# Performance work log

Measured on AMD Instinct MI355X. Metric: run time of the kernel, lower is better.

The kernel has to match this reference:

```python
import jax, jax.numpy as jnp
import numpy as np

B, S, E, H = 2, 2048, 1024, 16
D = E // H  # head_dim = 64


def setup_inputs() -> dict:
    key = jax.random.key(0)
    k1, k2, k3 = jax.random.split(key, 3)
    scale = 0.02  # GPT-2 init scale
    return {
        "hidden_states": jax.random.normal(k1, (B, S, E), dtype=jnp.float32),
        "c_attn_w": jax.random.normal(k2, (E, 3 * E), dtype=jnp.float32) * scale,
        "c_attn_b": jnp.zeros((3 * E,), dtype=jnp.float32),
        "c_proj_w": jax.random.normal(k3, (E, E), dtype=jnp.float32) * scale,
        "c_proj_b": jnp.zeros((E,), dtype=jnp.float32),
    }


def reference(hidden_states, c_attn_w, c_attn_b, c_proj_w, c_proj_b):
    # Conv1D: x @ W + b  -> qkv [B, S, 3E]
    qkv = hidden_states @ c_attn_w + c_attn_b
    q, k, v = jnp.split(qkv, 3, axis=-1)

    # split heads -> [B, H, S, D]
    def split_heads(t):
        return t.reshape(B, S, H, D).transpose(0, 2, 1, 3)

    q, k, v = split_heads(q), split_heads(k), split_heads(v)

    # naive full attention: QK^T / sqrt(D) -> softmax -> @ V
    attn_weights = jnp.einsum("bhqd,bhkd->bhqk", q, k) / jnp.sqrt(
        jnp.asarray(D, dtype=q.dtype)
    )
    attn_weights = jax.nn.softmax(attn_weights, axis=-1)
    attn_output = jnp.einsum("bhqk,bhkd->bhqd", attn_weights, v)

    # merge heads -> [B, S, E], then output projection
    attn_output = attn_output.transpose(0, 2, 1, 3).reshape(B, S, E)
    attn_output = attn_output @ c_proj_w + c_proj_b
    return attn_output
```

## Files before the change

kernel.cpp:

```cpp
#include <hip/hip_runtime.h>

#define SEQ 2048
#define EMB 1024
#define KDIM 1024
#define CF 0.180336880111113f

typedef __attribute__((ext_vector_type(8))) short short8_t;
typedef __attribute__((ext_vector_type(4))) float floatx4;
typedef __attribute__((ext_vector_type(4))) unsigned short ushort4_t;
typedef __attribute__((ext_vector_type(4))) unsigned int uivec4;

#define GLOAD16(gp, lp)                                                        \
  __builtin_amdgcn_global_load_lds(                                            \
      (const __attribute__((address_space(1))) void*)(gp),                     \
      (__attribute__((address_space(3))) void*)(lp), 16, 0, 0)

#define WGBAR()                                   \
  do {                                            \
    __asm__ __volatile__("" ::: "memory");        \
    __builtin_amdgcn_s_barrier();                 \
    __asm__ __volatile__("" ::: "memory");        \
  } while (0)

static __device__ __forceinline__ unsigned short f2bf(float x) {
  unsigned int u = __float_as_uint(x);
  return (unsigned short)((u + 0x7fffu + ((u >> 16) & 1u)) >> 16);
}

static __device__ __forceinline__ short8_t mk_pb(unsigned int a, unsigned int b,
                                                 unsigned int c, unsigned int d) {
  uivec4 t;
  t[0] = a; t[1] = b; t[2] = c; t[3] = d;
  return __builtin_bit_cast(short8_t, t);
}

static __device__ __forceinline__ unsigned int pack_bf(float p0, float p1) {
  return __builtin_amdgcn_perm(__float_as_uint(p1), __float_as_uint(p0),
                               0x07060302u);
}

static __device__ __forceinline__ void tconv_tile(
    const float* __restrict__ W, unsigned short* __restrict__ T, int N, int K,
    int n0, int k0, int tid) {
  __shared__ float Tl[64][65];
  const int lx = tid & 15, ly = tid >> 4;
#pragma unroll
  for (int u = 0; u < 4; ++u) {
    int r = u * 16 + ly;
    float4 v = *(const float4*)&W[(size_t)(k0 + r) * N + n0 + lx * 4];
    Tl[r][lx * 4 + 0] = v.x;
    Tl[r][lx * 4 + 1] = v.y;
    Tl[r][lx * 4 + 2] = v.z;
    Tl[r][lx * 4 + 3] = v.w;
  }
  __syncthreads();
#pragma unroll
  for (int u = 0; u < 4; ++u) {
    int n = u * 16 + ly;
    ushort4_t h;
#pragma unroll
    for (int v = 0; v < 4; ++v) h[v] = f2bf(Tl[lx * 4 + v][n]);
    *(ushort4_t*)&T[(size_t)(n0 + n) * K + k0 + lx * 4] = h;
  }
}

__global__ __launch_bounds__(256) void prep(
    const float* __restrict__ hs, const float* __restrict__ caw,
    const float* __restrict__ cpw, unsigned short* __restrict__ hsb,
    unsigned short* __restrict__ w1t, unsigned short* __restrict__ w2t) {
  const int bid = blockIdx.x, tid = threadIdx.x;
  if (bid < 4096) {
    const int i = bid * 256 + tid;
    float4 v = *(const float4*)&hs[(size_t)i * 4];
    ushort4_t h = {f2bf(v.x), f2bf(v.y), f2bf(v.z), f2bf(v.w)};
    *(ushort4_t*)&hsb[(size_t)i * 4] = h;
  } else if (bid < 4864) {
    const int idx = bid - 4096;
    tconv_tile(caw, w1t, 3 * EMB, EMB, (idx % 48) * 64, (idx / 48) * 64, tid);
  } else {
    const int idx = bid - 4864;
    tconv_tile(cpw, w2t, EMB, EMB, (idx % 16) * 64, (idx / 16) * 64, tid);
  }
}

template <int MODE, int BN>
__global__ __launch_bounds__(256, MODE == 0 ? 2 : 3) void gemm_pl(
    const unsigned short* __restrict__ Ag, const unsigned short* __restrict__ Bg,
    const float* __restrict__ bias, float* __restrict__ outF,
    unsigned short* __restrict__ qk, unsigned short* __restrict__ vt) {
  __shared__ __attribute__((aligned(16))) unsigned short Ah[2][128 * 64];
  __shared__ __attribute__((aligned(16))) unsigned short Bh[2][BN * 64];
  const int NJ = BN / 32;

  const int tid = threadIdx.x;
  const int w = tid >> 6, lane = tid & 63;
  const int quad = lane >> 4, c = lane & 15;
  const int rk = c & 7;

  int bm, bn;
  {
    const int L = blockIdx.x, x = L & 7, g = L >> 3;
    if (MODE == 0) {
      bm = ((x & 1) * 16 + (g & 15)) * 128;
      bn = ((x >> 1) * 6 + (g >> 4)) * 128;
    } else {
      bm = ((x & 3) * 8 + (g & 7)) * 128;
      bn = ((x >> 2) * 8 + (g >> 3)) * 64;
    }
  }
  const int wm = (w >> 1) * 64, wn = (w & 1) * (BN / 2);

  const unsigned short* gsrc = (w < 2) ? Ag : Bg;
  const int lbo = (w < 2) ? (w & 1) * 64 * 64 : (w & 1) * (BN / 2) * 64;
  const int rbase = (w < 2) ? (bm + (w & 1) * 64) : (bn + (w & 1) * (BN / 2));
  const int nloads = (w < 2) ? 8 : (BN / 16);
  const int srow = lane >> 3;
  const int sblkg = (lane & 7) ^ srow;
  const char* gp0 = (const char*)(gsrc + (size_t)(rbase + srow) * KDIM) + sblkg * 16;

  floatx4 acc[4][NJ];
  const floatx4 z = {0.f, 0.f, 0.f, 0.f};
#pragma unroll
  for (int i = 0; i < 4; ++i)
#pragma unroll
    for (int j = 0; j < NJ; ++j) acc[i][j] = z;

#define STAGE_G(buf, kt)                                                       \
  do {                                                                         \
    unsigned short* ld = ((w < 2) ? Ah[buf] : Bh[buf]) + lbo;                  \
    const char* gp = gp0 + (size_t)(kt) * 128;                                 \
    for (int i_ = 0; i_ < nloads; ++i_)                                        \
      GLOAD16(gp + (size_t)i_ * 8 * (KDIM * 2), &ld[i_ * 512]);                \
  } while (0)

  STAGE_G(0, 0);

  for (int t = 0; t < 16; ++t) {
    __asm__ __volatile__("s_waitcnt vmcnt(0)" ::: "memory");
    WGBAR();
    if (t < 15) STAGE_G((t + 1) & 1, t + 1);
    const unsigned short* Ac = Ah[t & 1];
    const unsigned short* Bc = Bh[t & 1];

#pragma unroll
    for (int kd = 0; kd < 2; ++kd) {
      const int oct = ((4 * kd + quad) ^ rk) * 8;
      short8_t a[4], b[NJ];
#pragma unroll
      for (int i = 0; i < 4; ++i)
        a[i] = *(const short8_t*)&Ac[(wm + 16 * i + c) * 64 + oct];
#pragma unroll
      for (int j = 0; j < NJ; ++j)
        b[j] = *(const short8_t*)&Bc[(wn + 16 * j + c) * 64 + oct];
#pragma unroll
      for (int i = 0; i < 4; ++i)
#pragma unroll
        for (int j = 0; j < NJ; ++j)
          acc[i][j] = __builtin_amdgcn_mfma_f32_16x16x32_bf16(b[j], a[i], acc[i][j], 0, 0, 0);
    }
  }
#undef STAGE_G

#pragma unroll
  for (int i = 0; i < 4; ++i) {
    const int row = bm + wm + 16 * i + c;
#pragma unroll
    for (int j = 0; j < NJ; ++j) {
      const int col0 = bn + wn + 16 * j + quad * 4;
      floatx4 v = acc[i][j] + *(const floatx4*)&bias[col0];
      if (MODE == 0) {
        if (col0 < 1024) v = v * CF;
        if (col0 < 2048) {
          ushort4_t pk = {f2bf(v[0]), f2bf(v[1]), f2bf(v[2]), f2bf(v[3])};
          *(ushort4_t*)&qk[(size_t)row * 2048 + col0] = pk;
        } else {
          const int c2 = col0 - 2048, hh = c2 >> 6, d0 = c2 & 63;
          const int bb = row >> 11, s = row & 2047;
          const int j = s & 63;
          const int lam = (j & 0x20) | ((j & 0x0C) << 1) | ((j & 0x10) >> 2) | (j & 3);
          const int sp = (s & ~63) | lam;
          unsigned short* vb = &vt[((size_t)(bb * 16 + hh) * 64 + d0) * 2048 + sp];
          vb[0 * 2048] = f2bf(v[0]);
          vb[1 * 2048] = f2bf(v[1]);
          vb[2 * 2048] = f2bf(v[2]);
          vb[3 * 2048] = f2bf(v[3]);
        }
      } else {
        *(floatx4*)&outF[(size_t)row * 1024 + col0] = v;
      }
    }
  }
}

static __device__ __forceinline__ void stage_kv16(
    int w, int srow, int sblkg, const unsigned short* __restrict__ gK,
    const unsigned short* __restrict__ gV, unsigned short* Kbuf,
    unsigned short* Vbuf, int jt) {
  if (w < 4) {
    const unsigned short* g0 =
        gK + (size_t)(jt * 64 + w * 16 + srow) * 2048 + sblkg * 8;
    unsigned short* l0 = &Kbuf[(w * 16) * 64];
    GLOAD16(g0, l0);
    GLOAD16(g0 + (size_t)8 * 2048, l0 + 8 * 64);
  } else {
    const unsigned short* g0 =
        gV + (size_t)((w - 4) * 16 + srow) * 2048 + jt * 64 + sblkg * 8;
    unsigned short* l0 = &Vbuf[((w - 4) * 16) * 64];
    GLOAD16(g0, l0);
    GLOAD16(g0 + (size_t)8 * 2048, l0 + 8 * 64);
  }
}

__global__ __launch_bounds__(512, 1) void attn10(
    const unsigned short* __restrict__ qk, const unsigned short* __restrict__ vt,
    unsigned short* __restrict__ ao) {
  __shared__ __attribute__((aligned(16))) unsigned short KV[6 * 4096];
  unsigned short* Ksb = KV;
  unsigned short* Vsb = KV + 3 * 4096;

  const int tid = threadIdx.x;
  const int w = tid >> 6, lane = tid & 63, quad = lane >> 4, c = lane & 15;
  const int qh = w >> 1, kh = w & 1;
  const int L = blockIdx.x, x = L & 7, g = L >> 3;
  const int hb = x * 4 + (g >> 3);
  const int h = hb & 15, b = hb >> 4;
  const int q0 = (g & 7) * 256;
  const int rk = c & 7;

  short8_t qf[4][2];
  {
    const size_t rb = (size_t)b * SEQ + q0 + qh * 64;
#pragma unroll
    for (int mi = 0; mi < 4; ++mi) {
      const size_t qr = (rb + mi * 16 + c) * 2048 + h * 64 + quad * 8;
      qf[mi][0] = *(const short8_t*)&qk[qr];
      qf[mi][1] = *(const short8_t*)&qk[qr + 32];
    }
  }
  __asm__ __volatile__("s_waitcnt vmcnt(0)" ::: "memory");

  floatx4 O[4][4], Osum[4];
  const floatx4 z = {0.f, 0.f, 0.f, 0.f};
#pragma unroll
  for (int mi = 0; mi < 4; ++mi) {
    Osum[mi] = z;
#pragma unroll
    for (int dg = 0; dg < 4; ++dg) O[mi][dg] = z;
  }
  short8_t ones;
#pragma unroll
  for (int e = 0; e < 8; ++e) ones[e] = (short)0x3F80;

  const int srow = lane >> 3;
  const int sblkg = (lane & 7) ^ srow;
  const unsigned short* gK = qk + (size_t)b * SEQ * 2048 + 1024 + h * 64;
  const unsigned short* gV = vt + (size_t)(b * 16 + h) * 64 * 2048;

  stage_kv16(w, srow, sblkg, gK, gV, Ksb, Vsb, 0);
  stage_kv16(w, srow, sblkg, gK, gV, Ksb + 4096, Vsb + 4096, 1);

  const int octv = ((4 * kh + quad) ^ rk) * 8;

  for (int t = 0; t < 32; ++t) {
    __asm__ __volatile__("s_waitcnt vmcnt(2)" ::: "memory");
    WGBAR();
    stage_kv16(w, srow, sblkg, gK, gV, Ksb + ((t + 2) % 3) * 4096,
               Vsb + ((t + 2) % 3) * 4096, (t + 2) & 31);
    const unsigned short* Kc = Ksb + (t % 3) * 4096;
    const unsigned short* Vc = Vsb + (t % 3) * 4096;

    floatx4 S[4][2];
#pragma unroll
    for (int mi = 0; mi < 4; ++mi)
#pragma unroll
      for (int jg = 0; jg < 2; ++jg) S[mi][jg] = z;
#pragma unroll
    for (int kd = 0; kd < 2; ++kd) {
      const int oct = ((4 * kd + quad) ^ rk) * 8;
#pragma unroll
      for (int jg = 0; jg < 2; ++jg) {
        short8_t kf = *(const short8_t*)&Kc[((kh * 2 + jg) * 16 + c) * 64 + oct];
#pragma unroll
        for (int mi = 0; mi < 4; ++mi)
          S[mi][jg] = __builtin_amdgcn_mfma_f32_16x16x32_bf16(kf, qf[mi][kd], S[mi][jg], 0, 0, 0);
      }
    }

#pragma unroll
    for (int mi = 0; mi < 4; ++mi) {
      unsigned int pw[2][2];
#pragma unroll
      for (int jg = 0; jg < 2; ++jg) {
        float p0 = __builtin_amdgcn_exp2f(S[mi][jg][0]);
        float p1 = __builtin_amdgcn_exp2f(S[mi][jg][1]);
        float p2 = __builtin_amdgcn_exp2f(S[mi][jg][2]);
        float p3 = __builtin_amdgcn_exp2f(S[mi][jg][3]);
        pw[jg][0] = pack_bf(p0, p1);
        pw[jg][1] = pack_bf(p2, p3);
      }
      short8_t pb = mk_pb(pw[0][0], pw[0][1], pw[1][0], pw[1][1]);
      Osum[mi] = __builtin_amdgcn_mfma_f32_16x16x32_bf16(ones, pb, Osum[mi], 0, 0, 0);
#pragma unroll
      for (int dg = 0; dg < 4; ++dg) {
        short8_t vf = *(const short8_t*)&Vc[(dg * 16 + c) * 64 + octv];
        O[mi][dg] = __builtin_amdgcn_mfma_f32_16x16x32_bf16(vf, pb, O[mi][dg], 0, 0, 0);
      }
    }
  }

  __asm__ __volatile__("s_waitcnt vmcnt(0)" ::: "memory");
  WGBAR();

  float* Of = (float*)KV;
  float* Ss2 = (float*)((char*)KV + 34816);
#pragma unroll
  for (int p = 0; p < 2; ++p) {
    if (kh == 1 && (qh >> 1) == p) {
#pragma unroll
      for (int mi = 0; mi < 4; ++mi) {
        const int row = (qh & 1) * 64 + mi * 16 + c;
        float* orow = &Of[row * 68];
#pragma unroll
        for (int dg = 0; dg < 4; ++dg)
          *(floatx4*)&orow[dg * 16 + quad * 4] = O[mi][dg];
        if (quad == 0) Ss2[row] = Osum[mi][0];
      }
    }
    WGBAR();
    if (kh == 0 && (qh >> 1) == p) {
#pragma unroll
      for (int mi = 0; mi < 4; ++mi) {
        const int row = (qh & 1) * 64 + mi * 16 + c;
        const float inv = 1.0f / (Osum[mi][0] + Ss2[row]);
        const float* orow = &Of[row * 68];
        const size_t grow = (size_t)b * SEQ + q0 + qh * 64 + mi * 16 + c;
#pragma unroll
        for (int dg = 0; dg < 4; ++dg) {
          floatx4 o = O[mi][dg] + *(const floatx4*)&orow[dg * 16 + quad * 4];
          ushort4_t ov = {f2bf(o[0] * inv), f2bf(o[1] * inv),
                          f2bf(o[2] * inv), f2bf(o[3] * inv)};
          *(ushort4_t*)&ao[grow * EMB + h * 64 + dg * 16 + quad * 4] = ov;
        }
      }
    }
    WGBAR();
  }
}

extern "C" void kernel_launch(void* const* d_in, const int* in_sizes, int n_in,
                              void* d_out, int out_size, void* d_ws, size_t ws_size,
                              hipStream_t stream) {
  const float* hs = (const float*)d_in[0];
  const float* c_attn_w = (const float*)d_in[1];
  const float* c_attn_b = (const float*)d_in[2];
  const float* c_proj_w = (const float*)d_in[3];
  const float* c_proj_b = (const float*)d_in[4];
  float* out = (float*)d_out;

  char* ws = (char*)d_ws;
  unsigned short* hsb = (unsigned short*)(ws + 0);
  unsigned short* qk  = (unsigned short*)(ws + 8388608);
  unsigned short* vt  = (unsigned short*)(ws + 25165824);
  unsigned short* aob = (unsigned short*)(ws + 33554432);
  unsigned short* w1t = (unsigned short*)(ws + 41943040);
  unsigned short* w2t = (unsigned short*)(ws + 48234496);

  prep<<<5120, 256, 0, stream>>>(hs, c_attn_w, c_proj_w, hsb, w1t, w2t);
  gemm_pl<0, 128><<<768, 256, 0, stream>>>(hsb, w1t, c_attn_b, nullptr, qk, vt);
  attn10<<<256, 512, 0, stream>>>(qk, vt, aob);
  gemm_pl<2, 64><<<512, 256, 0, stream>>>(aob, w2t, c_proj_b, out, nullptr, nullptr);
}
```

Before: 169.7 us.

## Give each warp private K staging and direct V register loads, removing block barriers

Restructures the attention kernel so each of the 8 warps owns 32 query rows and walks all keys on its own. Each warp streams K through a private triple-buffered LDS region and loads V straight from global memory into double-buffered registers. This removes the block-wide barriers and the cross-warp reduction of partial O and row sums at the end. In exchange, each warp fetches K and V itself, so global and L2 traffic per block goes up roughly eightfold, and the smaller per-warp MFMA tiles reuse each loaded K/V fragment less.

```diff
diff --git a/kernel.cpp b/kernel.cpp
--- a/kernel.cpp
+++ b/kernel.cpp
@@ -192,57 +192,32 @@
   }
 }
 
-static __device__ __forceinline__ void stage_kv16(
-    int w, int srow, int sblkg, const unsigned short* __restrict__ gK,
-    const unsigned short* __restrict__ gV, unsigned short* Kbuf,
-    unsigned short* Vbuf, int jt) {
-  if (w < 4) {
-    const unsigned short* g0 =
-        gK + (size_t)(jt * 64 + w * 16 + srow) * 2048 + sblkg * 8;
-    unsigned short* l0 = &Kbuf[(w * 16) * 64];
-    GLOAD16(g0, l0);
-    GLOAD16(g0 + (size_t)8 * 2048, l0 + 8 * 64);
-  } else {
-    const unsigned short* g0 =
-        gV + (size_t)((w - 4) * 16 + srow) * 2048 + jt * 64 + sblkg * 8;
-    unsigned short* l0 = &Vbuf[((w - 4) * 16) * 64];
-    GLOAD16(g0, l0);
-    GLOAD16(g0 + (size_t)8 * 2048, l0 + 8 * 64);
-  }
-}
-
-__global__ __launch_bounds__(512, 1) void attn10(
+__global__ __launch_bounds__(512, 1) void attn12(
     const unsigned short* __restrict__ qk, const unsigned short* __restrict__ vt,
     unsigned short* __restrict__ ao) {
-  __shared__ __attribute__((aligned(16))) unsigned short KV[6 * 4096];
-  unsigned short* Ksb = KV;
-  unsigned short* Vsb = KV + 3 * 4096;
+  __shared__ __attribute__((aligned(16))) unsigned short Kpriv[8 * 3 * 2048];
 
   const int tid = threadIdx.x;
   const int w = tid >> 6, lane = tid & 63, quad = lane >> 4, c = lane & 15;
-  const int qh = w >> 1, kh = w & 1;
   const int L = blockIdx.x, x = L & 7, g = L >> 3;
   const int hb = x * 4 + (g >> 3);
   const int h = hb & 15, b = hb >> 4;
-  const int q0 = (g & 7) * 256;
+  const int q0 = (g & 7) * 256 + w * 32;
   const int rk = c & 7;
 
-  short8_t qf[4][2];
-  {
-    const size_t rb = (size_t)b * SEQ + q0 + qh * 64;
-#pragma unroll
-    for (int mi = 0; mi < 4; ++mi) {
-      const size_t qr = (rb + mi * 16 + c) * 2048 + h * 64 + quad * 8;
-      qf[mi][0] = *(const short8_t*)&qk[qr];
-      qf[mi][1] = *(const short8_t*)&qk[qr + 32];
-    }
+  short8_t qf[2][2];
+#pragma unroll
+  for (int mi = 0; mi < 2; ++mi) {
+    const size_t qr = ((size_t)(b * SEQ + q0 + mi * 16 + c)) * 2048 + h * 64 + quad * 8;
+    qf[mi][0] = *(const short8_t*)&qk[qr];
+    qf[mi][1] = *(const short8_t*)&qk[qr + 32];
   }
   __asm__ __volatile__("s_waitcnt vmcnt(0)" ::: "memory");
 
-  floatx4 O[4][4], Osum[4];
+  floatx4 O[2][4], Osum[2];
   const floatx4 z = {0.f, 0.f, 0.f, 0.f};
 #pragma unroll
-  for (int mi = 0; mi < 4; ++mi) {
+  for (int mi = 0; mi < 2; ++mi) {
     Osum[mi] = z;
 #pragma unroll
     for (int dg = 0; dg < 4; ++dg) O[mi][dg] = z;
@@ -255,95 +230,95 @@
   const int sblkg = (lane & 7) ^ srow;
   const unsigned short* gK = qk + (size_t)b * SEQ * 2048 + 1024 + h * 64;
   const unsigned short* gV = vt + (size_t)(b * 16 + h) * 64 * 2048;
-
-  stage_kv16(w, srow, sblkg, gK, gV, Ksb, Vsb, 0);
-  stage_kv16(w, srow, sblkg, gK, gV, Ksb + 4096, Vsb + 4096, 1);
-
-  const int octv = ((4 * kh + quad) ^ rk) * 8;
-
-  for (int t = 0; t < 32; ++t) {
-    __asm__ __volatile__("s_waitcnt vmcnt(2)" ::: "memory");
-    WGBAR();
-    stage_kv16(w, srow, sblkg, gK, gV, Ksb + ((t + 2) % 3) * 4096,
-               Vsb + ((t + 2) % 3) * 4096, (t + 2) & 31);
-    const unsigned short* Kc = Ksb + (t % 3) * 4096;
-    const unsigned short* Vc = Vsb + (t % 3) * 4096;
-
-    floatx4 S[4][2];
-#pragma unroll
-    for (int mi = 0; mi < 4; ++mi)
-#pragma unroll
-      for (int jg = 0; jg < 2; ++jg) S[mi][jg] = z;
-#pragma unroll
-    for (int kd = 0; kd < 2; ++kd) {
-      const int oct = ((4 * kd + quad) ^ rk) * 8;
-#pragma unroll
-      for (int jg = 0; jg < 2; ++jg) {
-        short8_t kf = *(const short8_t*)&Kc[((kh * 2 + jg) * 16 + c) * 64 + oct];
-#pragma unroll
-        for (int mi = 0; mi < 4; ++mi)
-          S[mi][jg] = __builtin_amdgcn_mfma_f32_16x16x32_bf16(kf, qf[mi][kd], S[mi][jg], 0, 0, 0);
-      }
+  unsigned short* Kb = &Kpriv[w * 3 * 2048];
+
+#define STK(buf, t)                                                            \
+  do {                                                                         \
+    const unsigned short* g0_ = gK + (size_t)((t) * 32 + srow) * 2048 + sblkg * 8; \
+    unsigned short* l0_ = Kb + (buf) * 2048;                                   \
+    GLOAD16(g0_, l0_);                                                         \
+    GLOAD16(g0_ + (size_t)8 * 2048, l0_ + 512);                                \
+    GLOAD16(g0_ + (size_t)16 * 2048, l0_ + 1024);                              \
+    GLOAD16(g0_ + (size_t)24 * 2048, l0_ + 1536);                              \
+  } while (0)
+
+#define LDV(vf_, t)                                                            \
+  do {                                                                         \
+    _Pragma("unroll")                                                          \
+    for (int dg_ = 0; dg_ < 4; ++dg_)                                          \
+      vf_[dg_] = *(const short8_t*)&gV[(size_t)(dg_ * 16 + c) * 2048 +         \
+                                       (t) * 32 + quad * 8];                   \
+  } while (0)
+
+  short8_t vfA[4], vfB[4];
+  STK(0, 0);
+  __asm__ __volatile__("" ::: "memory");
+  LDV(vfA, 0);
+  __asm__ __volatile__("" ::: "memory");
+  STK(1, 1);
+
+#define ROUND(t, cur, nxt)                                                     \
+  do {                                                                         \
+    __asm__ __volatile__("s_waitcnt vmcnt(4)" ::: "memory");                   \
+    LDV(nxt, ((t) + 1) & 63);                                                  \
+    __asm__ __volatile__("" ::: "memory");                                     \
+    STK(((t) + 2) % 3, ((t) + 2) & 63);                                        \
+    __asm__ __volatile__("" ::: "memory");                                     \
+    const unsigned short* Kc = Kb + ((t) % 3) * 2048;                          \
+    floatx4 S[2][2];                                                           \
+    S[0][0] = z; S[0][1] = z; S[1][0] = z; S[1][1] = z;                        \
+    _Pragma("unroll")                                                          \
+    for (int kd = 0; kd < 2; ++kd) {                                           \
+      const int oct = ((4 * kd + quad) ^ rk) * 8;                              \
+      _Pragma("unroll")                                                        \
+      for (int jg = 0; jg < 2; ++jg) {                                         \
+        short8_t kf = *(const short8_t*)&Kc[(jg * 16 + c) * 64 + oct];         \
+        _Pragma("unroll")                                                      \
+        for (int mi = 0; mi < 2; ++mi)                                         \
+          S[mi][jg] = __builtin_amdgcn_mfma_f32_16x16x32_bf16(                 \
+              kf, qf[mi][kd], S[mi][jg], 0, 0, 0);                             \
+      }                                                                        \
+    }                                                                          \
+    _Pragma("unroll")                                                          \
+    for (int mi = 0; mi < 2; ++mi) {                                           \
+      unsigned int pw[2][2];                                                   \
+      _Pragma("unroll")                                                        \
+      for (int jg = 0; jg < 2; ++jg) {                                         \
+        float p0 = __builtin_amdgcn_exp2f(S[mi][jg][0]);                       \
+        float p1 = __builtin_amdgcn_exp2f(S[mi][jg][1]);                       \
+        float p2 = __builtin_amdgcn_exp2f(S[mi][jg][2]);                       \
+        float p3 = __builtin_amdgcn_exp2f(S[mi][jg][3]);                       \
+        pw[jg][0] = pack_bf(p0, p1);                                           \
+        pw[jg][1] = pack_bf(p2, p3);                                           \
+      }                                                                        \
+      short8_t pb = mk_pb(pw[0][0], pw[0][1], pw[1][0], pw[1][1]);             \
+      Osum[mi] = __builtin_amdgcn_mfma_f32_16x16x32_bf16(ones, pb, Osum[mi], 0, 0, 0); \
+      _Pragma("unroll")                                                        \
+      for (int dg = 0; dg < 4; ++dg)                                           \
+        O[mi][dg] = __builtin_amdgcn_mfma_f32_16x16x32_bf16(cur[dg], pb, O[mi][dg], 0, 0, 0); \
+    }                                                                          \
+  } while (0)
+
+  for (int t = 0; t < 64; t += 2) {
+    ROUND(t, vfA, vfB);
+    ROUND(t + 1, vfB, vfA);
+  }
+#undef ROUND
+#undef LDV
+#undef STK
+
+  __asm__ __volatile__("s_waitcnt vmcnt(0)" ::: "memory");
+
+#pragma unroll
+  for (int mi = 0; mi < 2; ++mi) {
+    const float inv = 1.0f / Osum[mi][0];
+    const size_t row = (size_t)b * SEQ + q0 + mi * 16 + c;
+#pragma unroll
+    for (int dg = 0; dg < 4; ++dg) {
+      ushort4_t ov = {f2bf(O[mi][dg][0] * inv), f2bf(O[mi][dg][1] * inv),
+                      f2bf(O[mi][dg][2] * inv), f2bf(O[mi][dg][3] * inv)};
+      *(ushort4_t*)&ao[row * EMB + h * 64 + dg * 16 + quad * 4] = ov;
     }
-
-#pragma unroll
-    for (int mi = 0; mi < 4; ++mi) {
-      unsigned int pw[2][2];
-#pragma unroll
-      for (int jg = 0; jg < 2; ++jg) {
-        float p0 = __builtin_amdgcn_exp2f(S[mi][jg][0]);
-        float p1 = __builtin_amdgcn_exp2f(S[mi][jg][1]);
-        float p2 = __builtin_amdgcn_exp2f(S[mi][jg][2]);
-        float p3 = __builtin_amdgcn_exp2f(S[mi][jg][3]);
-        pw[jg][0] = pack_bf(p0, p1);
-        pw[jg][1] = pack_bf(p2, p3);
-      }
-      short8_t pb = mk_pb(pw[0][0], pw[0][1], pw[1][0], pw[1][1]);
-      Osum[mi] = __builtin_amdgcn_mfma_f32_16x16x32_bf16(ones, pb, Osum[mi], 0, 0, 0);
-#pragma unroll
-      for (int dg = 0; dg < 4; ++dg) {
-        short8_t vf = *(const short8_t*)&Vc[(dg * 16 + c) * 64 + octv];
-        O[mi][dg] = __builtin_amdgcn_mfma_f32_16x16x32_bf16(vf, pb, O[mi][dg], 0, 0, 0);
-      }
-    }
-  }
-
-  __asm__ __volatile__("s_waitcnt vmcnt(0)" ::: "memory");
-  WGBAR();
-
-  float* Of = (float*)KV;
-  float* Ss2 = (float*)((char*)KV + 34816);
-#pragma unroll
-  for (int p = 0; p < 2; ++p) {
-    if (kh == 1 && (qh >> 1) == p) {
-#pragma unroll
-      for (int mi = 0; mi < 4; ++mi) {
-        const int row = (qh & 1) * 64 + mi * 16 + c;
-        float* orow = &Of[row * 68];
-#pragma unroll
-        for (int dg = 0; dg < 4; ++dg)
-          *(floatx4*)&orow[dg * 16 + quad * 4] = O[mi][dg];
-        if (quad == 0) Ss2[row] = Osum[mi][0];
-      }
-    }
-    WGBAR();
-    if (kh == 0 && (qh >> 1) == p) {
-#pragma unroll
-      for (int mi = 0; mi < 4; ++mi) {
-        const int row = (qh & 1) * 64 + mi * 16 + c;
-        const float inv = 1.0f / (Osum[mi][0] + Ss2[row]);
-        const float* orow = &Of[row * 68];
-        const size_t grow = (size_t)b * SEQ + q0 + qh * 64 + mi * 16 + c;
-#pragma unroll
-        for (int dg = 0; dg < 4; ++dg) {
-          floatx4 o = O[mi][dg] + *(const floatx4*)&orow[dg * 16 + quad * 4];
-          ushort4_t ov = {f2bf(o[0] * inv), f2bf(o[1] * inv),
-                          f2bf(o[2] * inv), f2bf(o[3] * inv)};
-          *(ushort4_t*)&ao[grow * EMB + h * 64 + dg * 16 + quad * 4] = ov;
-        }
-      }
-    }
-    WGBAR();
   }
 }
 
@@ -367,6 +342,6 @@
 
   prep<<<5120, 256, 0, stream>>>(hs, c_attn_w, c_proj_w, hsb, w1t, w2t);
   gemm_pl<0, 128><<<768, 256, 0, stream>>>(hsb, w1t, c_attn_b, nullptr, qk, vt);
-  attn10<<<256, 512, 0, stream>>>(qk, vt, aob);
+  attn12<<<256, 512, 0, stream>>>(qk, vt, aob);
   gemm_pl<2, 64><<<512, 256, 0, stream>>>(aob, w2t, c_proj_b, out, nullptr, nullptr);
 }
```

Measured after the change: 210.5 us. 1.24x slower.
